# Kernel tuning notes

Measured on AMD Instinct MI355X. Metric: run time of the kernel, lower is better.

## Reference

```python
import jax, jax.numpy as jnp
import numpy as np

N_NODES = 100000
N_EDGES = 1600000
N_GRAPHS = 1000
NODES_PER_GRAPH = N_NODES // N_GRAPHS
IN_DIM, HID_DIM, OUT_DIM = 32, 64, 32


def setup_inputs() -> dict:
    key = jax.random.key(0)
    k_x, k_src, k_dst, k_w1, k_w2 = jax.random.split(key, 5)
    x = jax.random.normal(k_x, (N_NODES, IN_DIM), dtype=jnp.float32)
    src = jax.random.randint(k_src, (N_EDGES,), 0, N_NODES, dtype=jnp.int32)
    dst = jax.random.randint(k_dst, (N_EDGES,), 0, N_NODES, dtype=jnp.int32)
    edge_index = jnp.stack([src, dst], axis=0)
    batch = (jnp.arange(N_NODES, dtype=jnp.int32) // NODES_PER_GRAPH)
    W1 = jax.random.normal(k_w1, (IN_DIM, HID_DIM), dtype=jnp.float32) / np.sqrt(IN_DIM)
    b1 = jnp.zeros((HID_DIM,), dtype=jnp.float32)
    W2 = jax.random.normal(k_w2, (HID_DIM, OUT_DIM), dtype=jnp.float32) / np.sqrt(HID_DIM)
    b2 = jnp.zeros((OUT_DIM,), dtype=jnp.float32)
    return {"x": x, "edge_index": edge_index, "batch": batch,
            "W1": W1, "b1": b1, "W2": W2, "b2": b2}


def _gcn_conv(x, W, b, src, dst, deg_inv_sqrt):
    # PyG GCNConv: out = D^{-1/2}(A+I)D^{-1/2} X W + b, deg includes self-loops
    h = x @ W  # [N, F]
    norm = deg_inv_sqrt[src] * deg_inv_sqrt[dst]  # [E]
    agg = jax.ops.segment_sum(h[src] * norm[:, None], dst, num_segments=N_NODES)
    # self-loop contribution: norm = deg^{-1/2} * deg^{-1/2} = 1/deg
    agg = agg + h * (deg_inv_sqrt * deg_inv_sqrt)[:, None]
    return agg + b


def reference(x, edge_index, batch, W1, b1, W2, b2):
    src, dst = edge_index[0], edge_index[1]
    # degree at target nodes, with self-loops
    deg = 1.0 + jax.ops.segment_sum(jnp.ones_like(dst, dtype=x.dtype), dst,
                                    num_segments=N_NODES)
    deg_inv_sqrt = jax.lax.rsqrt(deg)
    h = jax.nn.relu(_gcn_conv(x, W1, b1, src, dst, deg_inv_sqrt))
    h = _gcn_conv(h, W2, b2, src, dst, deg_inv_sqrt)
    # per-graph mean pooling (fused segment mean)
    sums = jax.ops.segment_sum(h, batch, num_segments=N_GRAPHS)
    counts = jax.ops.segment_sum(jnp.ones((h.shape[0],), dtype=h.dtype), batch,
                                 num_segments=N_GRAPHS)
    return sums / counts[:, None]
```

## Files before the change

kernel.cpp:

```cpp
#include <hip/hip_runtime.h>

#define IN_DIM 32
#define HID_DIM 64
#define OUT_DIM 32

#define WSHIFT 8
#define WMASK 255
#define MAXBUCK 512
#define CAP 5120
#define EPB 2048

typedef unsigned int u32;
typedef unsigned short u16;
typedef __attribute__((ext_vector_type(8))) short bf16x8;
typedef __attribute__((ext_vector_type(4))) float f32x4;

static __device__ __forceinline__ u32 bf16rne(float f) {
    u32 u = __float_as_uint(f);
    return (u + 0x7FFFu + ((u >> 16) & 1u)) >> 16;
}
static __device__ __forceinline__ float blo(u32 u) { return __uint_as_float(u << 16); }
static __device__ __forceinline__ float bhi(u32 u) { return __uint_as_float(u & 0xFFFF0000u); }

__global__ __launch_bounds__(256) void k_bin(const int* __restrict__ src,
                                             const int* __restrict__ dst,
                                             int* __restrict__ cursor,
                                             int* __restrict__ binned,
                                             int E, int nbuck) {
    __shared__ int lcnt[MAXBUCK];
    __shared__ int lbase[MAXBUCK];
    int t = threadIdx.x;
    lcnt[t] = 0; lcnt[t + 256] = 0;
    __syncthreads();
    int base = blockIdx.x * EPB;
    int dreg[8];
#pragma unroll
    for (int k = 0; k < 8; k++) {
        int e = base + k * 256 + t;
        dreg[k] = (e < E) ? dst[e] : -1;
    }
#pragma unroll
    for (int k = 0; k < 8; k++)
        if (dreg[k] >= 0) atomicAdd(&lcnt[dreg[k] >> WSHIFT], 1);
    __syncthreads();
    for (int b = t; b < nbuck; b += 256) {
        int c = lcnt[b];
        if (c) lbase[b] = atomicAdd(&cursor[b], c);
        lcnt[b] = 0;
    }
    __syncthreads();
#pragma unroll
    for (int k = 0; k < 8; k++) {
        int e = base + k * 256 + t;
        if (dreg[k] >= 0) {
            int d = dreg[k];
            int bk = d >> WSHIFT;
            int loc = lbase[bk] + atomicAdd(&lcnt[bk], 1);
            if (loc < CAP)
                binned[bk * CAP + loc] = ((d & WMASK) << 17) | src[e];
        }
    }
}

__global__ __launch_bounds__(256) void k_csr(const int* __restrict__ binned,
                                             const int* __restrict__ cursor,
                                             const float* __restrict__ x,
                                             int2* __restrict__ row,
                                             float* __restrict__ dis,
                                             u16* __restrict__ g,
                                             int* __restrict__ meta, int N) {
    __shared__ int sEdge[CAP];
    __shared__ int sH[4][256];
    __shared__ int sExcl[256];
    __shared__ int sCur[128];
    __shared__ float sdis[128];
    __shared__ int wsum[4];
    int bb = blockIdx.x;
    int b = bb >> 1;
    int h = bb & 1;
    int t = threadIdx.x;
    int wid = t >> 6;
    int s0 = b * CAP;
    int cnt = cursor[b];
    if (cnt > CAP) cnt = CAP;

    for (int k = t; k < 4 * 256; k += 256) ((int*)sH)[k] = 0;
    __syncthreads();

    for (int k = t; k < cnt; k += 256) {
        int p = binned[s0 + k];
        sEdge[k] = p;
        atomicAdd(&sH[wid][p >> 17], 1);
    }
    __syncthreads();

    int myv = sH[0][t] + sH[1][t] + sH[2][t] + sH[3][t];
    int lane = t & 63;
    int incl = myv;
#pragma unroll
    for (int o = 1; o < 64; o <<= 1) {
        int up = __shfl_up(incl, o);
        if (lane >= o) incl += up;
    }
    if (lane == 63) wsum[wid] = incl;
    sExcl[t] = incl - myv;
    if (t < 128) sCur[t] = 0;
    __syncthreads();
    int wpre = 0;
#pragma unroll
    for (int w = 0; w < 4; w++) wpre += (w < wid) ? wsum[w] : 0;
    int exclv = sExcl[t] + wpre;
    sExcl[t] = exclv;

    bool mine = ((t >> 7) == h);
    if (mine) {
        float d = rsqrtf(1.0f + (float)myv);
        sdis[t & 127] = d;
        int node = (b << WSHIFT) + t;
        if (node < N) {
            row[node] = make_int2(s0 + exclv, s0 + exclv + myv);
            dis[node] = d;
        }
    }
    __syncthreads();

    for (int k = t; k < cnt; k += 256) {
        int p = sEdge[k];
        int dl = p >> 17;
        if ((dl >> 7) == h) {
            int pos = sExcl[dl] + atomicAdd(&sCur[dl & 127], 1);
            meta[s0 + pos] = p & 0x1FFFF;
        }
    }

    int nbLo = (b << WSHIFT) + h * 128;
    int nn = N - nbLo;
    if (nn > 128) nn = 128;
    if (nn < 0) nn = 0;
    int halfE = nn * 16;
    const float* xb = x + (size_t)nbLo * 32;
    u32* gb = (u32*)(g + (size_t)nbLo * 32);
    for (int j = t; j < halfE; j += 256) {
        int e0 = j * 2;
        float dd = sdis[e0 >> 5];
        gb[j] = bf16rne(dd * xb[e0]) | (bf16rne(dd * xb[e0 + 1]) << 16);
    }
}

__global__ __launch_bounds__(256) void k_agg(const u16* __restrict__ g,
                                             const int* __restrict__ meta,
                                             const int2* __restrict__ row,
                                             const float* __restrict__ dis,
                                             u16* __restrict__ outf, int N) {
    int gid = blockIdx.x * 256 + threadIdx.x;
    int i = gid >> 5;
    if (i >= N) return;
    int l = threadIdx.x & 31;
    int grp = (l >> 2) & 7;
    int sub = l & 3;
    const uint4* gv = (const uint4*)g;

    float a0 = 0.f, a1 = 0.f, a2 = 0.f, a3 = 0.f;
    float a4 = 0.f, a5 = 0.f, a6 = 0.f, a7 = 0.f;
    int2 rw = row[i];
    int e = rw.x, end = rw.y;
    for (; e + 16 <= end; e += 16) {
        int s0 = meta[e + grp];
        int s1 = meta[e + 8 + grp];
        uint4 v0 = gv[s0 * 4 + sub];
        uint4 v1 = gv[s1 * 4 + sub];
        a0 += blo(v0.x); a1 += bhi(v0.x); a2 += blo(v0.y); a3 += bhi(v0.y);
        a4 += blo(v0.z); a5 += bhi(v0.z); a6 += blo(v0.w); a7 += bhi(v0.w);
        a0 += blo(v1.x); a1 += bhi(v1.x); a2 += blo(v1.y); a3 += bhi(v1.y);
        a4 += blo(v1.z); a5 += bhi(v1.z); a6 += blo(v1.w); a7 += bhi(v1.w);
    }
    if (e + grp < end) {
        uint4 v = gv[meta[e + grp] * 4 + sub];
        a0 += blo(v.x); a1 += bhi(v.x); a2 += blo(v.y); a3 += bhi(v.y);
        a4 += blo(v.z); a5 += bhi(v.z); a6 += blo(v.w); a7 += bhi(v.w);
    }
    if (e + 8 + grp < end) {
        uint4 v = gv[meta[e + 8 + grp] * 4 + sub];
        a0 += blo(v.x); a1 += bhi(v.x); a2 += blo(v.y); a3 += bhi(v.y);
        a4 += blo(v.z); a5 += bhi(v.z); a6 += blo(v.w); a7 += bhi(v.w);
    }
#pragma unroll
    for (int m = 4; m <= 16; m <<= 1) {
        a0 += __shfl_xor(a0, m); a1 += __shfl_xor(a1, m);
        a2 += __shfl_xor(a2, m); a3 += __shfl_xor(a3, m);
        a4 += __shfl_xor(a4, m); a5 += __shfl_xor(a5, m);
        a6 += __shfl_xor(a6, m); a7 += __shfl_xor(a7, m);
    }
    if (grp == 0) {
        uint4 sv = gv[i * 4 + sub];
        float d = dis[i];
        u32 o0 = bf16rne(d * (a0 + blo(sv.x))) | (bf16rne(d * (a1 + bhi(sv.x))) << 16);
        u32 o1 = bf16rne(d * (a2 + blo(sv.y))) | (bf16rne(d * (a3 + bhi(sv.y))) << 16);
        u32 o2 = bf16rne(d * (a4 + blo(sv.z))) | (bf16rne(d * (a5 + bhi(sv.z))) << 16);
        u32 o3 = bf16rne(d * (a6 + blo(sv.w))) | (bf16rne(d * (a7 + bhi(sv.w))) << 16);
        ((uint4*)outf)[i * 4 + sub] = make_uint4(o0, o1, o2, o3);
    }
}

__global__ __launch_bounds__(256) void k_mlp(const u16* __restrict__ aggX,
                                             const float* __restrict__ W1,
                                             const float* __restrict__ b1,
                                             const float* __restrict__ W2,
                                             const float* __restrict__ b2,
                                             const float* __restrict__ dis,
                                             u16* __restrict__ t2,
                                             float* __restrict__ out,
                                             int N, int outElems) {
    __shared__ float sHls[4][16 * 65];
    int t = threadIdx.x;
    int j = blockIdx.x * 256 + t;
    if (j < outElems) out[j] = b2[j & 31];

    int w = t >> 6;
    int L = t & 63;
    int q = L >> 4;
    int col = L & 15;
    int base = blockIdx.x * 64 + w * 16;

    int arow = base + col;
    uint4 av = (arow < N) ? ((const uint4*)aggX)[(size_t)arow * 4 + q]
                          : make_uint4(0, 0, 0, 0);
    bf16x8 afrag = *(bf16x8*)&av;

    bf16x8 b1f[4];
#pragma unroll
    for (int nt = 0; nt < 4; nt++) {
#pragma unroll
        for (int jj = 0; jj < 8; jj++)
            b1f[nt][jj] = (short)bf16rne(W1[(q * 8 + jj) * HID_DIM + nt * 16 + col]);
    }
    bf16x8 b2f[2][2];
#pragma unroll
    for (int ks = 0; ks < 2; ks++)
#pragma unroll
        for (int nt = 0; nt < 2; nt++) {
#pragma unroll
            for (int jj = 0; jj < 8; jj++)
                b2f[ks][nt][jj] =
                    (short)bf16rne(W2[(ks * 32 + q * 8 + jj) * OUT_DIM + nt * 16 + col]);
        }

#pragma unroll
    for (int nt = 0; nt < 4; nt++) {
        float bias = b1[nt * 16 + col];
        f32x4 c = {bias, bias, bias, bias};
        c = __builtin_amdgcn_mfma_f32_16x16x32_bf16(afrag, b1f[nt], c, 0, 0, 0);
#pragma unroll
        for (int r = 0; r < 4; r++)
            sHls[w][(q * 4 + r) * 65 + nt * 16 + col] = fmaxf(c[r], 0.0f);
    }
    __syncthreads();

    bf16x8 a2[2];
#pragma unroll
    for (int ks = 0; ks < 2; ks++) {
#pragma unroll
        for (int jj = 0; jj < 8; jj++)
            a2[ks][jj] = (short)bf16rne(sHls[w][col * 65 + ks * 32 + q * 8 + jj]);
    }

    f32x4 C2[2];
#pragma unroll
    for (int nt = 0; nt < 2; nt++) {
        f32x4 c = {0.f, 0.f, 0.f, 0.f};
        c = __builtin_amdgcn_mfma_f32_16x16x32_bf16(a2[0], b2f[0][nt], c, 0, 0, 0);
        c = __builtin_amdgcn_mfma_f32_16x16x32_bf16(a2[1], b2f[1][nt], c, 0, 0, 0);
        C2[nt] = c;
    }

#pragma unroll
    for (int r = 0; r < 4; r++) {
        int node = base + q * 4 + r;
        if (node < N) {
            float dd = dis[node];
            t2[(size_t)node * 32 + col]      = (u16)bf16rne(dd * C2[0][r]);
            t2[(size_t)node * 32 + 16 + col] = (u16)bf16rne(dd * C2[1][r]);
        }
    }
}

__global__ __launch_bounds__(256) void k_agg_pool(const u16* __restrict__ g,
                                                  const int* __restrict__ meta,
                                                  const int2* __restrict__ row,
                                                  const float* __restrict__ dis,
                                                  float* __restrict__ out,
                                                  int N, int npg, float inv_npg) {
    __shared__ float sval[8][32];
    int t = threadIdx.x;
    int hw = t >> 5;
    int base0 = blockIdx.x * 8;
    int i = base0 + hw;
    int l = t & 31;
    int grp = (l >> 2) & 7;
    int sub = l & 3;
    const uint4* gv = (const uint4*)g;

    float a0 = 0.f, a1 = 0.f, a2 = 0.f, a3 = 0.f;
    float a4 = 0.f, a5 = 0.f, a6 = 0.f, a7 = 0.f;
    bool valid = (i < N);
    if (valid) {
        int2 rw = row[i];
        int e = rw.x, end = rw.y;
        for (; e + 16 <= end; e += 16) {
            int s0 = meta[e + grp];
            int s1 = meta[e + 8 + grp];
            uint4 v0 = gv[s0 * 4 + sub];
            uint4 v1 = gv[s1 * 4 + sub];
            a0 += blo(v0.x); a1 += bhi(v0.x); a2 += blo(v0.y); a3 += bhi(v0.y);
            a4 += blo(v0.z); a5 += bhi(v0.z); a6 += blo(v0.w); a7 += bhi(v0.w);
            a0 += blo(v1.x); a1 += bhi(v1.x); a2 += blo(v1.y); a3 += bhi(v1.y);
            a4 += blo(v1.z); a5 += bhi(v1.z); a6 += blo(v1.w); a7 += bhi(v1.w);
        }
        if (e + grp < end) {
            uint4 v = gv[meta[e + grp] * 4 + sub];
            a0 += blo(v.x); a1 += bhi(v.x); a2 += blo(v.y); a3 += bhi(v.y);
            a4 += blo(v.z); a5 += bhi(v.z); a6 += blo(v.w); a7 += bhi(v.w);
        }
        if (e + 8 + grp < end) {
            uint4 v = gv[meta[e + 8 + grp] * 4 + sub];
            a0 += blo(v.x); a1 += bhi(v.x); a2 += blo(v.y); a3 += bhi(v.y);
            a4 += blo(v.z); a5 += bhi(v.z); a6 += blo(v.w); a7 += bhi(v.w);
        }
    }
#pragma unroll
    for (int m = 4; m <= 16; m <<= 1) {
        a0 += __shfl_xor(a0, m); a1 += __shfl_xor(a1, m);
        a2 += __shfl_xor(a2, m); a3 += __shfl_xor(a3, m);
        a4 += __shfl_xor(a4, m); a5 += __shfl_xor(a5, m);
        a6 += __shfl_xor(a6, m); a7 += __shfl_xor(a7, m);
    }
    if (grp == 0) {
        float4 r0 = make_float4(0.f, 0.f, 0.f, 0.f);
        float4 r1 = make_float4(0.f, 0.f, 0.f, 0.f);
        if (valid) {
            uint4 sv = gv[i * 4 + sub];
            float d = dis[i];
            r0.x = d * (a0 + blo(sv.x)); r0.y = d * (a1 + bhi(sv.x));
            r0.z = d * (a2 + blo(sv.y)); r0.w = d * (a3 + bhi(sv.y));
            r1.x = d * (a4 + blo(sv.z)); r1.y = d * (a5 + bhi(sv.z));
            r1.z = d * (a6 + blo(sv.w)); r1.w = d * (a7 + bhi(sv.w));
        }
        float4* sp = (float4*)&sval[hw][0];
        sp[sub * 2 + 0] = r0;
        sp[sub * 2 + 1] = r1;
    }
    __syncthreads();
    if (t < 32) {
        int gfirst = base0 / npg;
        int bound = (gfirst + 1) * npg;
        float acc = 0.0f;
        int curg = gfirst;
#pragma unroll
        for (int h = 0; h < 8; h++) {
            int node = base0 + h;
            if (node >= N) break;
            int gg = (node >= bound) ? gfirst + 1 : gfirst;
            if (gg != curg) {
                atomicAdd(&out[curg * 32 + t], acc * inv_npg);
                acc = 0.0f;
                curg = gg;
            }
            acc += sval[h][t];
        }
        atomicAdd(&out[curg * 32 + t], acc * inv_npg);
    }
}

extern "C" void kernel_launch(void* const* d_in, const int* in_sizes, int n_in,
                              void* d_out, int out_size, void* d_ws, size_t ws_size,
                              hipStream_t stream) {
    const float* x   = (const float*)d_in[0];
    const int* eidx  = (const int*)d_in[1];
    const float* W1  = (const float*)d_in[3];
    const float* b1  = (const float*)d_in[4];
    const float* W2  = (const float*)d_in[5];
    const float* b2  = (const float*)d_in[6];
    float* out       = (float*)d_out;

    const int N = in_sizes[0] / IN_DIM;
    const int E = in_sizes[1] / 2;
    const int G = out_size / OUT_DIM;
    const int npg = N / G;
    const int nbuck = (N + 255) >> WSHIFT;
    const int* src = eidx;
    const int* dst = eidx + E;

    char* ws = (char*)d_ws;
    size_t off = 0;
    auto alloc = [&](size_t bytes) -> char* {
        char* p = ws + off;
        off = (off + bytes + 255) & ~(size_t)255;
        return p;
    };
    int*   cursor = (int*)alloc(MAXBUCK * sizeof(int));
    int2*  row    = (int2*)alloc((size_t)N * sizeof(int2));
    float* dis    = (float*)alloc((size_t)N * sizeof(float));
    int*   binned = (int*)alloc((size_t)nbuck * CAP * sizeof(int));
    int*   meta   = (int*)alloc((size_t)nbuck * CAP * sizeof(int));
    u16*   g      = (u16*)alloc((size_t)N * IN_DIM * sizeof(u16));
    u16*   bufA   = (u16*)alloc((size_t)N * IN_DIM * sizeof(u16));
    u16*   bufB   = (u16*)alloc((size_t)N * OUT_DIM * sizeof(u16));
    (void)ws_size;

    hipMemsetAsync(cursor, 0, MAXBUCK * sizeof(int), stream);

    k_bin<<<(E + EPB - 1) / EPB, 256, 0, stream>>>(src, dst, cursor, binned, E, nbuck);
    k_csr<<<2 * nbuck, 256, 0, stream>>>(binned, cursor, x, row, dis, g, meta, N);
    k_agg<<<((size_t)N * 32 + 255) / 256, 256, 0, stream>>>(g, meta, row, dis, bufA, N);
    k_mlp<<<(N + 63) / 64, 256, 0, stream>>>(bufA, W1, b1, W2, b2, dis, bufB, out,
                                             N, G * OUT_DIM);
    k_agg_pool<<<(N + 7) / 8, 256, 0, stream>>>(bufB, meta, row, dis, out,
                                                N, npg, 1.0f / (float)npg);
}
```

Before: 189.5 us.

## Fuse first-layer neighbor aggregation into MLP kernel via shared memory

Merges the first aggregation kernel into the MLP kernel: each 256-thread block aggregates 64 nodes into LDS, then feeds them straight into the MFMA-based two-layer transform. This removes the intermediate bf16 buffer write and read and one kernel launch. In exchange each half-wave now processes 8 nodes in sequence and the grid is much smaller, which may reduce the memory-level parallelism available for the irregular gathers.

```diff
diff --git a/kernel.cpp b/kernel.cpp
--- a/kernel.cpp
+++ b/kernel.cpp
@@ -147,84 +147,87 @@
     }
 }
 
-__global__ __launch_bounds__(256) void k_agg(const u16* __restrict__ g,
-                                             const int* __restrict__ meta,
-                                             const int2* __restrict__ row,
-                                             const float* __restrict__ dis,
-                                             u16* __restrict__ outf, int N) {
-    int gid = blockIdx.x * 256 + threadIdx.x;
-    int i = gid >> 5;
-    if (i >= N) return;
-    int l = threadIdx.x & 31;
-    int grp = (l >> 2) & 7;
-    int sub = l & 3;
-    const uint4* gv = (const uint4*)g;
-
-    float a0 = 0.f, a1 = 0.f, a2 = 0.f, a3 = 0.f;
-    float a4 = 0.f, a5 = 0.f, a6 = 0.f, a7 = 0.f;
-    int2 rw = row[i];
-    int e = rw.x, end = rw.y;
-    for (; e + 16 <= end; e += 16) {
-        int s0 = meta[e + grp];
-        int s1 = meta[e + 8 + grp];
-        uint4 v0 = gv[s0 * 4 + sub];
-        uint4 v1 = gv[s1 * 4 + sub];
-        a0 += blo(v0.x); a1 += bhi(v0.x); a2 += blo(v0.y); a3 += bhi(v0.y);
-        a4 += blo(v0.z); a5 += bhi(v0.z); a6 += blo(v0.w); a7 += bhi(v0.w);
-        a0 += blo(v1.x); a1 += bhi(v1.x); a2 += blo(v1.y); a3 += bhi(v1.y);
-        a4 += blo(v1.z); a5 += bhi(v1.z); a6 += blo(v1.w); a7 += bhi(v1.w);
-    }
-    if (e + grp < end) {
-        uint4 v = gv[meta[e + grp] * 4 + sub];
-        a0 += blo(v.x); a1 += bhi(v.x); a2 += blo(v.y); a3 += bhi(v.y);
-        a4 += blo(v.z); a5 += bhi(v.z); a6 += blo(v.w); a7 += bhi(v.w);
-    }
-    if (e + 8 + grp < end) {
-        uint4 v = gv[meta[e + 8 + grp] * 4 + sub];
-        a0 += blo(v.x); a1 += bhi(v.x); a2 += blo(v.y); a3 += bhi(v.y);
-        a4 += blo(v.z); a5 += bhi(v.z); a6 += blo(v.w); a7 += bhi(v.w);
-    }
-#pragma unroll
-    for (int m = 4; m <= 16; m <<= 1) {
-        a0 += __shfl_xor(a0, m); a1 += __shfl_xor(a1, m);
-        a2 += __shfl_xor(a2, m); a3 += __shfl_xor(a3, m);
-        a4 += __shfl_xor(a4, m); a5 += __shfl_xor(a5, m);
-        a6 += __shfl_xor(a6, m); a7 += __shfl_xor(a7, m);
-    }
-    if (grp == 0) {
-        uint4 sv = gv[i * 4 + sub];
-        float d = dis[i];
-        u32 o0 = bf16rne(d * (a0 + blo(sv.x))) | (bf16rne(d * (a1 + bhi(sv.x))) << 16);
-        u32 o1 = bf16rne(d * (a2 + blo(sv.y))) | (bf16rne(d * (a3 + bhi(sv.y))) << 16);
-        u32 o2 = bf16rne(d * (a4 + blo(sv.z))) | (bf16rne(d * (a5 + bhi(sv.z))) << 16);
-        u32 o3 = bf16rne(d * (a6 + blo(sv.w))) | (bf16rne(d * (a7 + bhi(sv.w))) << 16);
-        ((uint4*)outf)[i * 4 + sub] = make_uint4(o0, o1, o2, o3);
-    }
-}
-
-__global__ __launch_bounds__(256) void k_mlp(const u16* __restrict__ aggX,
-                                             const float* __restrict__ W1,
-                                             const float* __restrict__ b1,
-                                             const float* __restrict__ W2,
-                                             const float* __restrict__ b2,
-                                             const float* __restrict__ dis,
-                                             u16* __restrict__ t2,
-                                             float* __restrict__ out,
-                                             int N, int outElems) {
+__global__ __launch_bounds__(256) void k_aggmlp(const u16* __restrict__ g,
+                                                const int* __restrict__ meta,
+                                                const int2* __restrict__ row,
+                                                const float* __restrict__ dis,
+                                                const float* __restrict__ W1,
+                                                const float* __restrict__ b1,
+                                                const float* __restrict__ W2,
+                                                const float* __restrict__ b2,
+                                                u16* __restrict__ t2,
+                                                float* __restrict__ out,
+                                                int N, int outElems) {
+    __shared__ u32 sA[64 * 16];
     __shared__ float sHls[4][16 * 65];
     int t = threadIdx.x;
     int j = blockIdx.x * 256 + t;
     if (j < outElems) out[j] = b2[j & 31];
+    int base = blockIdx.x * 64;
+
+    int hw = t >> 5;
+    int l = t & 31;
+    int grp = (l >> 2) & 7;
+    int sub = l & 3;
+    const uint4* gv = (const uint4*)g;
+
+    for (int n8 = 0; n8 < 8; n8++) {
+        int lid = hw * 8 + n8;
+        int i = base + lid;
+        float a0 = 0.f, a1 = 0.f, a2 = 0.f, a3 = 0.f;
+        float a4 = 0.f, a5 = 0.f, a6 = 0.f, a7 = 0.f;
+        if (i < N) {
+            int2 rw = row[i];
+            int e = rw.x, end = rw.y;
+            for (; e + 16 <= end; e += 16) {
+                int s0 = meta[e + grp];
+                int s1 = meta[e + 8 + grp];
+                uint4 v0 = gv[s0 * 4 + sub];
+                uint4 v1 = gv[s1 * 4 + sub];
+                a0 += blo(v0.x); a1 += bhi(v0.x); a2 += blo(v0.y); a3 += bhi(v0.y);
+                a4 += blo(v0.z); a5 += bhi(v0.z); a6 += blo(v0.w); a7 += bhi(v0.w);
+                a0 += blo(v1.x); a1 += bhi(v1.x); a2 += blo(v1.y); a3 += bhi(v1.y);
+                a4 += blo(v1.z); a5 += bhi(v1.z); a6 += blo(v1.w); a7 += bhi(v1.w);
+            }
+            if (e + grp < end) {
+                uint4 v = gv[meta[e + grp] * 4 + sub];
+                a0 += blo(v.x); a1 += bhi(v.x); a2 += blo(v.y); a3 += bhi(v.y);
+                a4 += blo(v.z); a5 += bhi(v.z); a6 += blo(v.w); a7 += bhi(v.w);
+            }
+            if (e + 8 + grp < end) {
+                uint4 v = gv[meta[e + 8 + grp] * 4 + sub];
+                a0 += blo(v.x); a1 += bhi(v.x); a2 += blo(v.y); a3 += bhi(v.y);
+                a4 += blo(v.z); a5 += bhi(v.z); a6 += blo(v.w); a7 += bhi(v.w);
+            }
+        }
+#pragma unroll
+        for (int m = 4; m <= 16; m <<= 1) {
+            a0 += __shfl_xor(a0, m); a1 += __shfl_xor(a1, m);
+            a2 += __shfl_xor(a2, m); a3 += __shfl_xor(a3, m);
+            a4 += __shfl_xor(a4, m); a5 += __shfl_xor(a5, m);
+            a6 += __shfl_xor(a6, m); a7 += __shfl_xor(a7, m);
+        }
+        if (grp == 0) {
+            uint4 pk = make_uint4(0, 0, 0, 0);
+            if (i < N) {
+                uint4 sv = gv[i * 4 + sub];
+                float d = dis[i];
+                pk.x = bf16rne(d * (a0 + blo(sv.x))) | (bf16rne(d * (a1 + bhi(sv.x))) << 16);
+                pk.y = bf16rne(d * (a2 + blo(sv.y))) | (bf16rne(d * (a3 + bhi(sv.y))) << 16);
+                pk.z = bf16rne(d * (a4 + blo(sv.z))) | (bf16rne(d * (a5 + bhi(sv.z))) << 16);
+                pk.w = bf16rne(d * (a6 + blo(sv.w))) | (bf16rne(d * (a7 + bhi(sv.w))) << 16);
+            }
+            ((uint4*)sA)[lid * 4 + sub] = pk;
+        }
+    }
+    __syncthreads();
 
     int w = t >> 6;
     int L = t & 63;
     int q = L >> 4;
     int col = L & 15;
-    int base = blockIdx.x * 64 + w * 16;
-
-    int arow = base + col;
-    uint4 av = (arow < N) ? ((const uint4*)aggX)[(size_t)arow * 4 + q]
-                          : make_uint4(0, 0, 0, 0);
+
+    uint4 av = ((uint4*)sA)[(w * 16 + col) * 4 + q];
     bf16x8 afrag = *(bf16x8*)&av;
 
     bf16x8 b1f[4];
@@ -275,7 +278,7 @@
 
 #pragma unroll
     for (int r = 0; r < 4; r++) {
-        int node = base + q * 4 + r;
+        int node = base + w * 16 + q * 4 + r;
         if (node < N) {
             float dd = dis[node];
             t2[(size_t)node * 32 + col]      = (u16)bf16rne(dd * C2[0][r]);
@@ -403,7 +406,6 @@
     int*   binned = (int*)alloc((size_t)nbuck * CAP * sizeof(int));
     int*   meta   = (int*)alloc((size_t)nbuck * CAP * sizeof(int));
     u16*   g      = (u16*)alloc((size_t)N * IN_DIM * sizeof(u16));
-    u16*   bufA   = (u16*)alloc((size_t)N * IN_DIM * sizeof(u16));
     u16*   bufB   = (u16*)alloc((size_t)N * OUT_DIM * sizeof(u16));
     (void)ws_size;
 
@@ -411,9 +413,8 @@
 
     k_bin<<<(E + EPB - 1) / EPB, 256, 0, stream>>>(src, dst, cursor, binned, E, nbuck);
     k_csr<<<2 * nbuck, 256, 0, stream>>>(binned, cursor, x, row, dis, g, meta, N);
-    k_agg<<<((size_t)N * 32 + 255) / 256, 256, 0, stream>>>(g, meta, row, dis, bufA, N);
-    k_mlp<<<(N + 63) / 64, 256, 0, stream>>>(bufA, W1, b1, W2, b2, dis, bufB, out,
-                                             N, G * OUT_DIM);
+    k_aggmlp<<<(N + 63) / 64, 256, 0, stream>>>(g, meta, row, dis, W1, b1, W2, b2,
+                                                bufB, out, N, G * OUT_DIM);
     k_agg_pool<<<(N + 7) / 8, 256, 0, stream>>>(bufB, meta, row, dis, out,
                                                 N, npg, 1.0f / (float)npg);
 }
```

After: 205.6 us. 1.08x slower.

## Fuse all stages into one persistent cooperative kernel with grid syncs

Applied to the files above, without the earlier changes.

Replaces the memset and five separate kernel launches (bin, CSR build, first aggregation, MLP, second aggregation with pooling) with a single cooperative persistent kernel. Blocks loop over virtual block indices and stages are separated by grid-wide barriers. Shared memory is a union of the per-stage buffers. The aim is to remove launch gaps and per-kernel tail effects, at the cost of grid-sync overhead, a grid capped at occupancy times 256, and possibly lower occupancy from the largest shared-memory footprint (CSR stage, about 26KB).

```diff
diff --git a/kernel.cpp b/kernel.cpp
--- a/kernel.cpp
+++ b/kernel.cpp
@@ -1,4 +1,7 @@
 #include <hip/hip_runtime.h>
+#include <hip/hip_cooperative_groups.h>
+
+namespace cg = cooperative_groups;
 
 #define IN_DIM 32
 #define HID_DIM 64
@@ -22,352 +25,356 @@
 static __device__ __forceinline__ float blo(u32 u) { return __uint_as_float(u << 16); }
 static __device__ __forceinline__ float bhi(u32 u) { return __uint_as_float(u & 0xFFFF0000u); }
 
-__global__ __launch_bounds__(256) void k_bin(const int* __restrict__ src,
-                                             const int* __restrict__ dst,
-                                             int* __restrict__ cursor,
-                                             int* __restrict__ binned,
-                                             int E, int nbuck) {
-    __shared__ int lcnt[MAXBUCK];
-    __shared__ int lbase[MAXBUCK];
+struct MegaArgs {
+    const int* src; const int* dst; const float* x;
+    const float* W1; const float* b1; const float* W2; const float* b2;
+    int* cursor; int2* row; float* dis; int* binned; int* meta;
+    u16* g; u16* bufA; u16* bufB; float* out;
+    int N, E, nbuck, npg, outElems;
+    float inv_npg;
+};
+
+union SMem {
+    struct { int lcnt[MAXBUCK]; int lbase[MAXBUCK]; } bin;
+    struct { int sEdge[CAP]; int sH[4][256]; int sExcl[256];
+             int sCur[128]; float sdis[128]; int wsum[4]; } csr;
+    struct { float sHls[4][16 * 65]; } mlp;
+    struct { float sval[8][32]; } pool;
+};
+
+__global__ __launch_bounds__(256, 4) void k_mega(MegaArgs A) {
+    cg::grid_group gridg = cg::this_grid();
+    __shared__ SMem sm;
     int t = threadIdx.x;
-    lcnt[t] = 0; lcnt[t + 256] = 0;
-    __syncthreads();
-    int base = blockIdx.x * EPB;
-    int dreg[8];
-#pragma unroll
-    for (int k = 0; k < 8; k++) {
-        int e = base + k * 256 + t;
-        dreg[k] = (e < E) ? dst[e] : -1;
+    int nB = gridDim.x;
+
+    for (int i = blockIdx.x * 256 + t; i < MAXBUCK; i += nB * 256) A.cursor[i] = 0;
+    gridg.sync();
+
+    int nbinb = (A.E + EPB - 1) / EPB;
+    for (int vb = blockIdx.x; vb < nbinb; vb += nB) {
+        sm.bin.lcnt[t] = 0; sm.bin.lcnt[t + 256] = 0;
+        __syncthreads();
+        int base = vb * EPB;
+        int dreg[8];
+#pragma unroll
+        for (int k = 0; k < 8; k++) {
+            int e = base + k * 256 + t;
+            dreg[k] = (e < A.E) ? A.dst[e] : -1;
+        }
+#pragma unroll
+        for (int k = 0; k < 8; k++)
+            if (dreg[k] >= 0) atomicAdd(&sm.bin.lcnt[dreg[k] >> WSHIFT], 1);
+        __syncthreads();
+        for (int b = t; b < A.nbuck; b += 256) {
+            int c = sm.bin.lcnt[b];
+            if (c) sm.bin.lbase[b] = atomicAdd(&A.cursor[b], c);
+            sm.bin.lcnt[b] = 0;
+        }
+        __syncthreads();
+#pragma unroll
+        for (int k = 0; k < 8; k++) {
+            int e = base + k * 256 + t;
+            if (dreg[k] >= 0) {
+                int d = dreg[k];
+                int bk = d >> WSHIFT;
+                int loc = sm.bin.lbase[bk] + atomicAdd(&sm.bin.lcnt[bk], 1);
+                if (loc < CAP)
+                    A.binned[bk * CAP + loc] = ((d & WMASK) << 17) | A.src[e];
+            }
+        }
+        __syncthreads();
     }
-#pragma unroll
-    for (int k = 0; k < 8; k++)
-        if (dreg[k] >= 0) atomicAdd(&lcnt[dreg[k] >> WSHIFT], 1);
-    __syncthreads();
-    for (int b = t; b < nbuck; b += 256) {
-        int c = lcnt[b];
-        if (c) lbase[b] = atomicAdd(&cursor[b], c);
-        lcnt[b] = 0;
+    gridg.sync();
+
+    for (int vb = blockIdx.x; vb < 2 * A.nbuck; vb += nB) {
+        int b = vb >> 1;
+        int h = vb & 1;
+        int wid = t >> 6;
+        int s0 = b * CAP;
+        int cnt = A.cursor[b];
+        if (cnt > CAP) cnt = CAP;
+
+        for (int k = t; k < 4 * 256; k += 256) ((int*)sm.csr.sH)[k] = 0;
+        __syncthreads();
+
+        for (int k = t; k < cnt; k += 256) {
+            int p = A.binned[s0 + k];
+            sm.csr.sEdge[k] = p;
+            atomicAdd(&sm.csr.sH[wid][p >> 17], 1);
+        }
+        __syncthreads();
+
+        int myv = sm.csr.sH[0][t] + sm.csr.sH[1][t] + sm.csr.sH[2][t] + sm.csr.sH[3][t];
+        int lane = t & 63;
+        int incl = myv;
+#pragma unroll
+        for (int o = 1; o < 64; o <<= 1) {
+            int up = __shfl_up(incl, o);
+            if (lane >= o) incl += up;
+        }
+        if (lane == 63) sm.csr.wsum[wid] = incl;
+        sm.csr.sExcl[t] = incl - myv;
+        if (t < 128) sm.csr.sCur[t] = 0;
+        __syncthreads();
+        int wpre = 0;
+#pragma unroll
+        for (int w = 0; w < 4; w++) wpre += (w < wid) ? sm.csr.wsum[w] : 0;
+        int exclv = sm.csr.sExcl[t] + wpre;
+        sm.csr.sExcl[t] = exclv;
+
+        bool mine = ((t >> 7) == h);
+        if (mine) {
+            float d = rsqrtf(1.0f + (float)myv);
+            sm.csr.sdis[t & 127] = d;
+            int node = (b << WSHIFT) + t;
+            if (node < A.N) {
+                A.row[node] = make_int2(s0 + exclv, s0 + exclv + myv);
+                A.dis[node] = d;
+            }
+        }
+        __syncthreads();
+
+        for (int k = t; k < cnt; k += 256) {
+            int p = sm.csr.sEdge[k];
+            int dl = p >> 17;
+            if ((dl >> 7) == h) {
+                int pos = sm.csr.sExcl[dl] + atomicAdd(&sm.csr.sCur[dl & 127], 1);
+                A.meta[s0 + pos] = p & 0x1FFFF;
+            }
+        }
+
+        int nbLo = (b << WSHIFT) + h * 128;
+        int nn = A.N - nbLo;
+        if (nn > 128) nn = 128;
+        if (nn < 0) nn = 0;
+        int halfE = nn * 16;
+        const float* xb = A.x + (size_t)nbLo * 32;
+        u32* gb = (u32*)(A.g + (size_t)nbLo * 32);
+        for (int j = t; j < halfE; j += 256) {
+            int e0 = j * 2;
+            float dd = sm.csr.sdis[e0 >> 5];
+            gb[j] = bf16rne(dd * xb[e0]) | (bf16rne(dd * xb[e0 + 1]) << 16);
+        }
+        __syncthreads();
     }
-    __syncthreads();
-#pragma unroll
-    for (int k = 0; k < 8; k++) {
-        int e = base + k * 256 + t;
-        if (dreg[k] >= 0) {
-            int d = dreg[k];
-            int bk = d >> WSHIFT;
-            int loc = lbase[bk] + atomicAdd(&lcnt[bk], 1);
-            if (loc < CAP)
-                binned[bk * CAP + loc] = ((d & WMASK) << 17) | src[e];
+    gridg.sync();
+
+    {
+        int hw5 = t >> 5;
+        int l = t & 31;
+        int grp = (l >> 2) & 7;
+        int sub = l & 3;
+        const uint4* gv = (const uint4*)A.g;
+        int naggb = (A.N * 32 + 255) / 256;
+        for (int vb = blockIdx.x; vb < naggb; vb += nB) {
+            int i = vb * 8 + hw5;
+            float a0 = 0.f, a1 = 0.f, a2 = 0.f, a3 = 0.f;
+            float a4 = 0.f, a5 = 0.f, a6 = 0.f, a7 = 0.f;
+            if (i < A.N) {
+                int2 rw = A.row[i];
+                int e = rw.x, end = rw.y;
+                for (; e + 16 <= end; e += 16) {
+                    int s0 = A.meta[e + grp];
+                    int s1 = A.meta[e + 8 + grp];
+                    uint4 v0 = gv[s0 * 4 + sub];
+                    uint4 v1 = gv[s1 * 4 + sub];
+                    a0 += blo(v0.x); a1 += bhi(v0.x); a2 += blo(v0.y); a3 += bhi(v0.y);
+                    a4 += blo(v0.z); a5 += bhi(v0.z); a6 += blo(v0.w); a7 += bhi(v0.w);
+                    a0 += blo(v1.x); a1 += bhi(v1.x); a2 += blo(v1.y); a3 += bhi(v1.y);
+                    a4 += blo(v1.z); a5 += bhi(v1.z); a6 += blo(v1.w); a7 += bhi(v1.w);
+                }
+                if (e + grp < end) {
+                    uint4 v = gv[A.meta[e + grp] * 4 + sub];
+                    a0 += blo(v.x); a1 += bhi(v.x); a2 += blo(v.y); a3 += bhi(v.y);
+                    a4 += blo(v.z); a5 += bhi(v.z); a6 += blo(v.w); a7 += bhi(v.w);
+                }
+                if (e + 8 + grp < end) {
+                    uint4 v = gv[A.meta[e + 8 + grp] * 4 + sub];
+                    a0 += blo(v.x); a1 += bhi(v.x); a2 += blo(v.y); a3 += bhi(v.y);
+                    a4 += blo(v.z); a5 += bhi(v.z); a6 += blo(v.w); a7 += bhi(v.w);
+                }
+            }
+#pragma unroll
+            for (int m = 4; m <= 16; m <<= 1) {
+                a0 += __shfl_xor(a0, m); a1 += __shfl_xor(a1, m);
+                a2 += __shfl_xor(a2, m); a3 += __shfl_xor(a3, m);
+                a4 += __shfl_xor(a4, m); a5 += __shfl_xor(a5, m);
+                a6 += __shfl_xor(a6, m); a7 += __shfl_xor(a7, m);
+            }
+            if (grp == 0 && i < A.N) {
+                uint4 sv = gv[i * 4 + sub];
+                float d = A.dis[i];
+                u32 o0 = bf16rne(d * (a0 + blo(sv.x))) | (bf16rne(d * (a1 + bhi(sv.x))) << 16);
+                u32 o1 = bf16rne(d * (a2 + blo(sv.y))) | (bf16rne(d * (a3 + bhi(sv.y))) << 16);
+                u32 o2 = bf16rne(d * (a4 + blo(sv.z))) | (bf16rne(d * (a5 + bhi(sv.z))) << 16);
+                u32 o3 = bf16rne(d * (a6 + blo(sv.w))) | (bf16rne(d * (a7 + bhi(sv.w))) << 16);
+                ((uint4*)A.bufA)[i * 4 + sub] = make_uint4(o0, o1, o2, o3);
+            }
         }
     }
-}
-
-__global__ __launch_bounds__(256) void k_csr(const int* __restrict__ binned,
-                                             const int* __restrict__ cursor,
-                                             const float* __restrict__ x,
-                                             int2* __restrict__ row,
-                                             float* __restrict__ dis,
-                                             u16* __restrict__ g,
-                                             int* __restrict__ meta, int N) {
-    __shared__ int sEdge[CAP];
-    __shared__ int sH[4][256];
-    __shared__ int sExcl[256];
-    __shared__ int sCur[128];
-    __shared__ float sdis[128];
-    __shared__ int wsum[4];
-    int bb = blockIdx.x;
-    int b = bb >> 1;
-    int h = bb & 1;
-    int t = threadIdx.x;
-    int wid = t >> 6;
-    int s0 = b * CAP;
-    int cnt = cursor[b];
-    if (cnt > CAP) cnt = CAP;
-
-    for (int k = t; k < 4 * 256; k += 256) ((int*)sH)[k] = 0;
-    __syncthreads();
-
-    for (int k = t; k < cnt; k += 256) {
-        int p = binned[s0 + k];
-        sEdge[k] = p;
-        atomicAdd(&sH[wid][p >> 17], 1);
+    gridg.sync();
+
+    {
+        int w = t >> 6;
+        int L = t & 63;
+        int q = L >> 4;
+        int col = L & 15;
+
+        bf16x8 b1f[4];
+#pragma unroll
+        for (int nt = 0; nt < 4; nt++) {
+#pragma unroll
+            for (int jj = 0; jj < 8; jj++)
+                b1f[nt][jj] = (short)bf16rne(A.W1[(q * 8 + jj) * HID_DIM + nt * 16 + col]);
+        }
+        bf16x8 b2f[2][2];
+#pragma unroll
+        for (int ks = 0; ks < 2; ks++)
+#pragma unroll
+            for (int nt = 0; nt < 2; nt++) {
+#pragma unroll
+                for (int jj = 0; jj < 8; jj++)
+                    b2f[ks][nt][jj] =
+                        (short)bf16rne(A.W2[(ks * 32 + q * 8 + jj) * OUT_DIM + nt * 16 + col]);
+            }
+        float bias[4];
+#pragma unroll
+        for (int nt = 0; nt < 4; nt++) bias[nt] = A.b1[nt * 16 + col];
+
+        int nmlpb = (A.N + 63) / 64;
+        for (int vb = blockIdx.x; vb < nmlpb; vb += nB) {
+            int j = vb * 256 + t;
+            if (j < A.outElems) A.out[j] = A.b2[j & 31];
+            int base = vb * 64;
+
+            int arow = base + w * 16 + col;
+            uint4 av = (arow < A.N) ? ((const uint4*)A.bufA)[(size_t)arow * 4 + q]
+                                    : make_uint4(0, 0, 0, 0);
+            bf16x8 afrag = *(bf16x8*)&av;
+
+#pragma unroll
+            for (int nt = 0; nt < 4; nt++) {
+                f32x4 c = {bias[nt], bias[nt], bias[nt], bias[nt]};
+                c = __builtin_amdgcn_mfma_f32_16x16x32_bf16(afrag, b1f[nt], c, 0, 0, 0);
+#pragma unroll
+                for (int r = 0; r < 4; r++)
+                    sm.mlp.sHls[w][(q * 4 + r) * 65 + nt * 16 + col] = fmaxf(c[r], 0.0f);
+            }
+            __syncthreads();
+
+            bf16x8 a2[2];
+#pragma unroll
+            for (int ks = 0; ks < 2; ks++) {
+#pragma unroll
+                for (int jj = 0; jj < 8; jj++)
+                    a2[ks][jj] = (short)bf16rne(sm.mlp.sHls[w][col * 65 + ks * 32 + q * 8 + jj]);
+            }
+
+            f32x4 C2[2];
+#pragma unroll
+            for (int nt = 0; nt < 2; nt++) {
+                f32x4 c = {0.f, 0.f, 0.f, 0.f};
+                c = __builtin_amdgcn_mfma_f32_16x16x32_bf16(a2[0], b2f[0][nt], c, 0, 0, 0);
+                c = __builtin_amdgcn_mfma_f32_16x16x32_bf16(a2[1], b2f[1][nt], c, 0, 0, 0);
+                C2[nt] = c;
+            }
+
+#pragma unroll
+            for (int r = 0; r < 4; r++) {
+                int node = base + w * 16 + q * 4 + r;
+                if (node < A.N) {
+                    float dd = A.dis[node];
+                    A.bufB[(size_t)node * 32 + col]      = (u16)bf16rne(dd * C2[0][r]);
+                    A.bufB[(size_t)node * 32 + 16 + col] = (u16)bf16rne(dd * C2[1][r]);
+                }
+            }
+            __syncthreads();
+        }
     }
-    __syncthreads();
-
-    int myv = sH[0][t] + sH[1][t] + sH[2][t] + sH[3][t];
-    int lane = t & 63;
-    int incl = myv;
-#pragma unroll
-    for (int o = 1; o < 64; o <<= 1) {
-        int up = __shfl_up(incl, o);
-        if (lane >= o) incl += up;
-    }
-    if (lane == 63) wsum[wid] = incl;
-    sExcl[t] = incl - myv;
-    if (t < 128) sCur[t] = 0;
-    __syncthreads();
-    int wpre = 0;
-#pragma unroll
-    for (int w = 0; w < 4; w++) wpre += (w < wid) ? wsum[w] : 0;
-    int exclv = sExcl[t] + wpre;
-    sExcl[t] = exclv;
-
-    bool mine = ((t >> 7) == h);
-    if (mine) {
-        float d = rsqrtf(1.0f + (float)myv);
-        sdis[t & 127] = d;
-        int node = (b << WSHIFT) + t;
-        if (node < N) {
-            row[node] = make_int2(s0 + exclv, s0 + exclv + myv);
-            dis[node] = d;
-        }
-    }
-    __syncthreads();
-
-    for (int k = t; k < cnt; k += 256) {
-        int p = sEdge[k];
-        int dl = p >> 17;
-        if ((dl >> 7) == h) {
-            int pos = sExcl[dl] + atomicAdd(&sCur[dl & 127], 1);
-            meta[s0 + pos] = p & 0x1FFFF;
-        }
-    }
-
-    int nbLo = (b << WSHIFT) + h * 128;
-    int nn = N - nbLo;
-    if (nn > 128) nn = 128;
-    if (nn < 0) nn = 0;
-    int halfE = nn * 16;
-    const float* xb = x + (size_t)nbLo * 32;
-    u32* gb = (u32*)(g + (size_t)nbLo * 32);
-    for (int j = t; j < halfE; j += 256) {
-        int e0 = j * 2;
-        float dd = sdis[e0 >> 5];
-        gb[j] = bf16rne(dd * xb[e0]) | (bf16rne(dd * xb[e0 + 1]) << 16);
-    }
-}
-
-__global__ __launch_bounds__(256) void k_agg(const u16* __restrict__ g,
-                                             const int* __restrict__ meta,
-                                             const int2* __restrict__ row,
-                                             const float* __restrict__ dis,
-                                             u16* __restrict__ outf, int N) {
-    int gid = blockIdx.x * 256 + threadIdx.x;
-    int i = gid >> 5;
-    if (i >= N) return;
-    int l = threadIdx.x & 31;
-    int grp = (l >> 2) & 7;
-    int sub = l & 3;
-    const uint4* gv = (const uint4*)g;
-
-    float a0 = 0.f, a1 = 0.f, a2 = 0.f, a3 = 0.f;
-    float a4 = 0.f, a5 = 0.f, a6 = 0.f, a7 = 0.f;
-    int2 rw = row[i];
-    int e = rw.x, end = rw.y;
-    for (; e + 16 <= end; e += 16) {
-        int s0 = meta[e + grp];
-        int s1 = meta[e + 8 + grp];
-        uint4 v0 = gv[s0 * 4 + sub];
-        uint4 v1 = gv[s1 * 4 + sub];
-        a0 += blo(v0.x); a1 += bhi(v0.x); a2 += blo(v0.y); a3 += bhi(v0.y);
-        a4 += blo(v0.z); a5 += bhi(v0.z); a6 += blo(v0.w); a7 += bhi(v0.w);
-        a0 += blo(v1.x); a1 += bhi(v1.x); a2 += blo(v1.y); a3 += bhi(v1.y);
-        a4 += blo(v1.z); a5 += bhi(v1.z); a6 += blo(v1.w); a7 += bhi(v1.w);
-    }
-    if (e + grp < end) {
-        uint4 v = gv[meta[e + grp] * 4 + sub];
-        a0 += blo(v.x); a1 += bhi(v.x); a2 += blo(v.y); a3 += bhi(v.y);
-        a4 += blo(v.z); a5 += bhi(v.z); a6 += blo(v.w); a7 += bhi(v.w);
-    }
-    if (e + 8 + grp < end) {
-        uint4 v = gv[meta[e + 8 + grp] * 4 + sub];
-        a0 += blo(v.x); a1 += bhi(v.x); a2 += blo(v.y); a3 += bhi(v.y);
-        a4 += blo(v.z); a5 += bhi(v.z); a6 += blo(v.w); a7 += bhi(v.w);
-    }
-#pragma unroll
-    for (int m = 4; m <= 16; m <<= 1) {
-        a0 += __shfl_xor(a0, m); a1 += __shfl_xor(a1, m);
-        a2 += __shfl_xor(a2, m); a3 += __shfl_xor(a3, m);
-        a4 += __shfl_xor(a4, m); a5 += __shfl_xor(a5, m);
-        a6 += __shfl_xor(a6, m); a7 += __shfl_xor(a7, m);
-    }
-    if (grp == 0) {
-        uint4 sv = gv[i * 4 + sub];
-        float d = dis[i];
-        u32 o0 = bf16rne(d * (a0 + blo(sv.x))) | (bf16rne(d * (a1 + bhi(sv.x))) << 16);
-        u32 o1 = bf16rne(d * (a2 + blo(sv.y))) | (bf16rne(d * (a3 + bhi(sv.y))) << 16);
-        u32 o2 = bf16rne(d * (a4 + blo(sv.z))) | (bf16rne(d * (a5 + bhi(sv.z))) << 16);
-        u32 o3 = bf16rne(d * (a6 + blo(sv.w))) | (bf16rne(d * (a7 + bhi(sv.w))) << 16);
-        ((uint4*)outf)[i * 4 + sub] = make_uint4(o0, o1, o2, o3);
-    }
-}
-
-__global__ __launch_bounds__(256) void k_mlp(const u16* __restrict__ aggX,
-                                             const float* __restrict__ W1,
-                                             const float* __restrict__ b1,
-                                             const float* __restrict__ W2,
-                                             const float* __restrict__ b2,
-                                             const float* __restrict__ dis,
-                                             u16* __restrict__ t2,
-                                             float* __restrict__ out,
-                                             int N, int outElems) {
-    __shared__ float sHls[4][16 * 65];
-    int t = threadIdx.x;
-    int j = blockIdx.x * 256 + t;
-    if (j < outElems) out[j] = b2[j & 31];
-
-    int w = t >> 6;
-    int L = t & 63;
-    int q = L >> 4;
-    int col = L & 15;
-    int base = blockIdx.x * 64 + w * 16;
-
-    int arow = base + col;
-    uint4 av = (arow < N) ? ((const uint4*)aggX)[(size_t)arow * 4 + q]
-                          : make_uint4(0, 0, 0, 0);
-    bf16x8 afrag = *(bf16x8*)&av;
-
-    bf16x8 b1f[4];
-#pragma unroll
-    for (int nt = 0; nt < 4; nt++) {
-#pragma unroll
-        for (int jj = 0; jj < 8; jj++)
-            b1f[nt][jj] = (short)bf16rne(W1[(q * 8 + jj) * HID_DIM + nt * 16 + col]);
-    }
-    bf16x8 b2f[2][2];
-#pragma unroll
-    for (int ks = 0; ks < 2; ks++)
-#pragma unroll
-        for (int nt = 0; nt < 2; nt++) {
-#pragma unroll
-            for (int jj = 0; jj < 8; jj++)
-                b2f[ks][nt][jj] =
-                    (short)bf16rne(W2[(ks * 32 + q * 8 + jj) * OUT_DIM + nt * 16 + col]);
-        }
-
-#pragma unroll
-    for (int nt = 0; nt < 4; nt++) {
-        float bias = b1[nt * 16 + col];
-        f32x4 c = {bias, bias, bias, bias};
-        c = __builtin_amdgcn_mfma_f32_16x16x32_bf16(afrag, b1f[nt], c, 0, 0, 0);
-#pragma unroll
-        for (int r = 0; r < 4; r++)
-            sHls[w][(q * 4 + r) * 65 + nt * 16 + col] = fmaxf(c[r], 0.0f);
-    }
-    __syncthreads();
-
-    bf16x8 a2[2];
-#pragma unroll
-    for (int ks = 0; ks < 2; ks++) {
-#pragma unroll
-        for (int jj = 0; jj < 8; jj++)
-            a2[ks][jj] = (short)bf16rne(sHls[w][col * 65 + ks * 32 + q * 8 + jj]);
-    }
-
-    f32x4 C2[2];
-#pragma unroll
-    for (int nt = 0; nt < 2; nt++) {
-        f32x4 c = {0.f, 0.f, 0.f, 0.f};
-        c = __builtin_amdgcn_mfma_f32_16x16x32_bf16(a2[0], b2f[0][nt], c, 0, 0, 0);
-        c = __builtin_amdgcn_mfma_f32_16x16x32_bf16(a2[1], b2f[1][nt], c, 0, 0, 0);
-        C2[nt] = c;
-    }
-
-#pragma unroll
-    for (int r = 0; r < 4; r++) {
-        int node = base + q * 4 + r;
-        if (node < N) {
-            float dd = dis[node];
-            t2[(size_t)node * 32 + col]      = (u16)bf16rne(dd * C2[0][r]);
-            t2[(size_t)node * 32 + 16 + col] = (u16)bf16rne(dd * C2[1][r]);
-        }
-    }
-}
-
-__global__ __launch_bounds__(256) void k_agg_pool(const u16* __restrict__ g,
-                                                  const int* __restrict__ meta,
-                                                  const int2* __restrict__ row,
-                                                  const float* __restrict__ dis,
-                                                  float* __restrict__ out,
-                                                  int N, int npg, float inv_npg) {
-    __shared__ float sval[8][32];
-    int t = threadIdx.x;
-    int hw = t >> 5;
-    int base0 = blockIdx.x * 8;
-    int i = base0 + hw;
-    int l = t & 31;
-    int grp = (l >> 2) & 7;
-    int sub = l & 3;
-    const uint4* gv = (const uint4*)g;
-
-    float a0 = 0.f, a1 = 0.f, a2 = 0.f, a3 = 0.f;
-    float a4 = 0.f, a5 = 0.f, a6 = 0.f, a7 = 0.f;
-    bool valid = (i < N);
-    if (valid) {
-        int2 rw = row[i];
-        int e = rw.x, end = rw.y;
-        for (; e + 16 <= end; e += 16) {
-            int s0 = meta[e + grp];
-            int s1 = meta[e + 8 + grp];
-            uint4 v0 = gv[s0 * 4 + sub];
-            uint4 v1 = gv[s1 * 4 + sub];
-            a0 += blo(v0.x); a1 += bhi(v0.x); a2 += blo(v0.y); a3 += bhi(v0.y);
-            a4 += blo(v0.z); a5 += bhi(v0.z); a6 += blo(v0.w); a7 += bhi(v0.w);
-            a0 += blo(v1.x); a1 += bhi(v1.x); a2 += blo(v1.y); a3 += bhi(v1.y);
-            a4 += blo(v1.z); a5 += bhi(v1.z); a6 += blo(v1.w); a7 += bhi(v1.w);
-        }
-        if (e + grp < end) {
-            uint4 v = gv[meta[e + grp] * 4 + sub];
-            a0 += blo(v.x); a1 += bhi(v.x); a2 += blo(v.y); a3 += bhi(v.y);
-            a4 += blo(v.z); a5 += bhi(v.z); a6 += blo(v.w); a7 += bhi(v.w);
-        }
-        if (e + 8 + grp < end) {
-            uint4 v = gv[meta[e + 8 + grp] * 4 + sub];
-            a0 += blo(v.x); a1 += bhi(v.x); a2 += blo(v.y); a3 += bhi(v.y);
-            a4 += blo(v.z); a5 += bhi(v.z); a6 += blo(v.w); a7 += bhi(v.w);
-        }
-    }
-#pragma unroll
-    for (int m = 4; m <= 16; m <<= 1) {
-        a0 += __shfl_xor(a0, m); a1 += __shfl_xor(a1, m);
-        a2 += __shfl_xor(a2, m); a3 += __shfl_xor(a3, m);
-        a4 += __shfl_xor(a4, m); a5 += __shfl_xor(a5, m);
-        a6 += __shfl_xor(a6, m); a7 += __shfl_xor(a7, m);
-    }
-    if (grp == 0) {
-        float4 r0 = make_float4(0.f, 0.f, 0.f, 0.f);
-        float4 r1 = make_float4(0.f, 0.f, 0.f, 0.f);
-        if (valid) {
-            uint4 sv = gv[i * 4 + sub];
-            float d = dis[i];
-            r0.x = d * (a0 + blo(sv.x)); r0.y = d * (a1 + bhi(sv.x));
-            r0.z = d * (a2 + blo(sv.y)); r0.w = d * (a3 + bhi(sv.y));
-            r1.x = d * (a4 + blo(sv.z)); r1.y = d * (a5 + bhi(sv.z));
-            r1.z = d * (a6 + blo(sv.w)); r1.w = d * (a7 + bhi(sv.w));
-        }
-        float4* sp = (float4*)&sval[hw][0];
-        sp[sub * 2 + 0] = r0;
-        sp[sub * 2 + 1] = r1;
-    }
-    __syncthreads();
-    if (t < 32) {
-        int gfirst = base0 / npg;
-        int bound = (gfirst + 1) * npg;
-        float acc = 0.0f;
-        int curg = gfirst;
-#pragma unroll
-        for (int h = 0; h < 8; h++) {
-            int node = base0 + h;
-            if (node >= N) break;
-            int gg = (node >= bound) ? gfirst + 1 : gfirst;
-            if (gg != curg) {
-                atomicAdd(&out[curg * 32 + t], acc * inv_npg);
-                acc = 0.0f;
-                curg = gg;
-            }
-            acc += sval[h][t];
-        }
-        atomicAdd(&out[curg * 32 + t], acc * inv_npg);
+    gridg.sync();
+
+    {
+        int hw = t >> 5;
+        int l = t & 31;
+        int grp = (l >> 2) & 7;
+        int sub = l & 3;
+        const uint4* gv = (const uint4*)A.bufB;
+        int npoolb = (A.N + 7) / 8;
+        for (int vb = blockIdx.x; vb < npoolb; vb += nB) {
+            int base0 = vb * 8;
+            int i = base0 + hw;
+            float a0 = 0.f, a1 = 0.f, a2 = 0.f, a3 = 0.f;
+            float a4 = 0.f, a5 = 0.f, a6 = 0.f, a7 = 0.f;
+            bool valid = (i < A.N);
+            if (valid) {
+                int2 rw = A.row[i];
+                int e = rw.x, end = rw.y;
+                for (; e + 16 <= end; e += 16) {
+                    int s0 = A.meta[e + grp];
+                    int s1 = A.meta[e + 8 + grp];
+                    uint4 v0 = gv[s0 * 4 + sub];
+                    uint4 v1 = gv[s1 * 4 + sub];
+                    a0 += blo(v0.x); a1 += bhi(v0.x); a2 += blo(v0.y); a3 += bhi(v0.y);
+                    a4 += blo(v0.z); a5 += bhi(v0.z); a6 += blo(v0.w); a7 += bhi(v0.w);
+                    a0 += blo(v1.x); a1 += bhi(v1.x); a2 += blo(v1.y); a3 += bhi(v1.y);
+                    a4 += blo(v1.z); a5 += bhi(v1.z); a6 += blo(v1.w); a7 += bhi(v1.w);
+                }
+                if (e + grp < end) {
+                    uint4 v = gv[A.meta[e + grp] * 4 + sub];
+                    a0 += blo(v.x); a1 += bhi(v.x); a2 += blo(v.y); a3 += bhi(v.y);
+                    a4 += blo(v.z); a5 += bhi(v.z); a6 += blo(v.w); a7 += bhi(v.w);
+                }
+                if (e + 8 + grp < end) {
+                    uint4 v = gv[A.meta[e + 8 + grp] * 4 + sub];
+                    a0 += blo(v.x); a1 += bhi(v.x); a2 += blo(v.y); a3 += bhi(v.y);
+                    a4 += blo(v.z); a5 += bhi(v.z); a6 += blo(v.w); a7 += bhi(v.w);
+                }
+            }
+#pragma unroll
+            for (int m = 4; m <= 16; m <<= 1) {
+                a0 += __shfl_xor(a0, m); a1 += __shfl_xor(a1, m);
+                a2 += __shfl_xor(a2, m); a3 += __shfl_xor(a3, m);
+                a4 += __shfl_xor(a4, m); a5 += __shfl_xor(a5, m);
+                a6 += __shfl_xor(a6, m); a7 += __shfl_xor(a7, m);
+            }
+            if (grp == 0) {
+                float4 r0 = make_float4(0.f, 0.f, 0.f, 0.f);
+                float4 r1 = make_float4(0.f, 0.f, 0.f, 0.f);
+                if (valid) {
+                    uint4 sv = gv[i * 4 + sub];
+                    float d = A.dis[i];
+                    r0.x = d * (a0 + blo(sv.x)); r0.y = d * (a1 + bhi(sv.x));
+                    r0.z = d * (a2 + blo(sv.y)); r0.w = d * (a3 + bhi(sv.y));
+                    r1.x = d * (a4 + blo(sv.z)); r1.y = d * (a5 + bhi(sv.z));
+                    r1.z = d * (a6 + blo(sv.w)); r1.w = d * (a7 + bhi(sv.w));
+                }
+                float4* sp = (float4*)&sm.pool.sval[hw][0];
+                sp[sub * 2 + 0] = r0;
+                sp[sub * 2 + 1] = r1;
+            }
+            __syncthreads();
+            if (t < 32) {
+                int gfirst = base0 / A.npg;
+                int bound = (gfirst + 1) * A.npg;
+                float acc = 0.0f;
+                int curg = gfirst;
+#pragma unroll
+                for (int hh = 0; hh < 8; hh++) {
+                    int node = base0 + hh;
+                    if (node >= A.N) break;
+                    int gg2 = (node >= bound) ? gfirst + 1 : gfirst;
+                    if (gg2 != curg) {
+                        atomicAdd(&A.out[curg * 32 + t], acc * A.inv_npg);
+                        acc = 0.0f;
+                        curg = gg2;
+                    }
+                    acc += sm.pool.sval[hh][t];
+                }
+                atomicAdd(&A.out[curg * 32 + t], acc * A.inv_npg);
+            }
+            __syncthreads();
+        }
     }
 }
 
@@ -387,8 +394,6 @@
     const int G = out_size / OUT_DIM;
     const int npg = N / G;
     const int nbuck = (N + 255) >> WSHIFT;
-    const int* src = eidx;
-    const int* dst = eidx + E;
 
     char* ws = (char*)d_ws;
     size_t off = 0;
@@ -407,13 +412,22 @@
     u16*   bufB   = (u16*)alloc((size_t)N * OUT_DIM * sizeof(u16));
     (void)ws_size;
 
-    hipMemsetAsync(cursor, 0, MAXBUCK * sizeof(int), stream);
-
-    k_bin<<<(E + EPB - 1) / EPB, 256, 0, stream>>>(src, dst, cursor, binned, E, nbuck);
-    k_csr<<<2 * nbuck, 256, 0, stream>>>(binned, cursor, x, row, dis, g, meta, N);
-    k_agg<<<((size_t)N * 32 + 255) / 256, 256, 0, stream>>>(g, meta, row, dis, bufA, N);
-    k_mlp<<<(N + 63) / 64, 256, 0, stream>>>(bufA, W1, b1, W2, b2, dis, bufB, out,
-                                             N, G * OUT_DIM);
-    k_agg_pool<<<(N + 7) / 8, 256, 0, stream>>>(bufB, meta, row, dis, out,
-                                                N, npg, 1.0f / (float)npg);
+    MegaArgs A;
+    A.src = eidx; A.dst = eidx + E; A.x = x;
+    A.W1 = W1; A.b1 = b1; A.W2 = W2; A.b2 = b2;
+    A.cursor = cursor; A.row = row; A.dis = dis; A.binned = binned; A.meta = meta;
+    A.g = g; A.bufA = bufA; A.bufB = bufB; A.out = out;
+    A.N = N; A.E = E; A.nbuck = nbuck; A.npg = npg;
+    A.outElems = G * OUT_DIM; A.inv_npg = 1.0f / (float)npg;
+
+    int maxBpc = 0;
+    hipError_t err = hipOccupancyMaxActiveBlocksPerMultiprocessor(
+        &maxBpc, (const void*)k_mega, 256, 0);
+    if (err != hipSuccess || maxBpc < 1) maxBpc = 2;
+    if (maxBpc > 8) maxBpc = 8;
+    int grid = maxBpc * 256;
+
+    void* args[] = { (void*)&A };
+    hipLaunchCooperativeKernel((const void*)k_mega, dim3(grid), dim3(256),
+                               args, 0, stream);
 }
```

After: 691.4 us. +264.8%, slower.
